# Kernel tuning notes

Measured on AMD Instinct MI355X. Metric: run time of the kernel, lower is better.

Reference implementation:

```python
import jax, jax.numpy as jnp
import numpy as np

BLANK = 512  # blank label index (= vocab_size, last slot of V+1 logits)


def setup_inputs() -> dict:
    key = jax.random.key(0)
    k1, k2, k3, k4 = jax.random.split(key, 4)
    B, T, U, V1 = 16, 256, 64, 513
    logits = jax.random.normal(k1, (B, T, U + 1, V1), dtype=jnp.float32)
    logit_lens = jax.random.randint(k2, (B,), T // 2, T + 1, dtype=jnp.int32)
    y = jax.random.randint(k3, (B, U), 0, BLANK, dtype=jnp.int32)  # labels != blank
    y_lens = jax.random.randint(k4, (B,), U // 2, U + 1, dtype=jnp.int32)
    return {"logits": logits, "logit_lens": logit_lens, "y": y, "y_lens": y_lens}


def _per_seq_loss(logits, y, T_len, U_len):
    # logits: [T, U+1, V+1]; y: [U]
    logp = jax.nn.log_softmax(logits, axis=-1)
    blank_lp = logp[..., BLANK]                                   # [T, U+1]
    # label emission log-prob at (t, u) for emitting y[u]:
    lab_lp = jnp.take_along_axis(logp[:, :-1, :], y[None, :, None], axis=-1)[..., 0]  # [T, U]
    zero = jnp.zeros((1,), logp.dtype)

    def cum(lab_row):
        # c[u] = sum_{j<u} lab_row[j], length U+1
        return jnp.concatenate([zero, jnp.cumsum(lab_row)])

    # alpha recurrence: alpha[t,u] = logaddexp(alpha[t-1,u] + blank_lp[t-1,u],
    #                                          alpha[t,u-1] + lab_lp[t,u-1])
    # Within a row t the u-recursion a[u] = logaddexp(base[u], a[u-1]+lab[u-1])
    # has closed form a[u] = c[u] + logcumsumexp(base - c)[u].
    row0 = cum(lab_lp[0])  # alpha[0, u] = sum of label lps along u axis at t=0

    def step(prev, xs):
        blank_row, lab_row = xs
        base = prev + blank_row          # contribution from alpha[t-1, u]
        c = cum(lab_row)
        a = c + jax.lax.cumlogsumexp(base - c)
        return a, a

    _, rows = jax.lax.scan(step, row0, (blank_lp[:-1], lab_lp[1:]))
    alphas = jnp.concatenate([row0[None], rows], axis=0)  # [T, U+1]
    # final blank transition from (T_len-1, U_len)
    ll = alphas[T_len - 1, U_len] + blank_lp[T_len - 1, U_len]
    return -ll


def reference(logits, logit_lens, y, y_lens):
    per_seq = jax.vmap(_per_seq_loss)(logits, y, logit_lens, y_lens)
    return jnp.mean(per_seq)  # warprnnt 'mean' reduction: average over batch
```

## Files before the change

kernel.cpp:

```cpp
#include <hip/hip_runtime.h>
#include <math.h>

#define BATCH 16
#define TMAX  256
#define UU    64
#define U1    65
#define V1    513
#define BLANKI 512
#define NEG_INF (-INFINITY)

#define BLK_PAD  64
#define LAB_PAD  64
#define BLK_ROWS 384
#define LAB_ROWS 392
#define BLK_SLAB (BLK_ROWS * U1)
#define LAB_SLAB (LAB_ROWS * UU)
#define LOSS_OFF 0
#define BLK_OFF  16
#define LAB_OFF  (BLK_OFF + BATCH * BLK_SLAB)

__device__ __forceinline__ float lae(float x, float y) {
    float m = fmaxf(x, y);
    float z = fminf(x, y);
    return m + __logf(1.0f + __expf(z - m));
}

__global__ __launch_bounds__(1024) void lse_kernel(const float* __restrict__ logits,
                                                   const int* __restrict__ y,
                                                   const int* __restrict__ logit_lens,
                                                   const int* __restrict__ y_lens,
                                                   float* __restrict__ ws) {
    const int wave = (int)((blockIdx.x * 1024u + threadIdx.x) >> 6);
    const int lane = threadIdx.x & 63;
    const int ncells = BATCH * TMAX * U1;
    if (wave >= ncells) return;

    const int u  = wave % U1;
    const int bt = wave / U1;
    const int b  = bt / TMAX;
    const int t  = bt - b * TMAX;
    if (t >= logit_lens[b] || u > y_lens[b]) return;

    const long long base = (long long)wave * V1;

    float v[8];
#pragma unroll
    for (int k = 0; k < 8; ++k) v[k] = logits[base + lane + (k << 6)];
    float vb = (lane == 0) ? logits[base + BLANKI] : NEG_INF;

    float m = vb;
#pragma unroll
    for (int k = 0; k < 8; ++k) m = fmaxf(m, v[k]);
#pragma unroll
    for (int off = 32; off; off >>= 1) m = fmaxf(m, __shfl_xor(m, off));

    float s = (lane == 0) ? __expf(vb - m) : 0.0f;
#pragma unroll
    for (int k = 0; k < 8; ++k) s += __expf(v[k] - m);
#pragma unroll
    for (int off = 32; off; off >>= 1) s += __shfl_xor(s, off);

    const float lse = m + __logf(s);

    if (lane == 0) {
        float* blk = ws + BLK_OFF + b * BLK_SLAB + BLK_PAD * U1;
        blk[t * U1 + u] = vb - lse;
        if (u < UU) {
            float* lab = ws + LAB_OFF + b * LAB_SLAB + LAB_PAD * UU;
            const int label = y[b * UU + u];
            lab[t * UU + u] = logits[base + label] - lse;
        }
    }
}

__global__ __launch_bounds__(64) void alpha_kernel(const float* __restrict__ ws,
                                                   const int* __restrict__ logit_lens,
                                                   const int* __restrict__ y_lens,
                                                   float* __restrict__ losses) {
    const int b    = blockIdx.x;
    const int lane = threadIdx.x;

    const float* __restrict__ blk = ws + BLK_OFF + b * BLK_SLAB + BLK_PAD * U1;
    const float* __restrict__ lab = ws + LAB_OFF + b * LAB_SLAB + LAB_PAD * UU;
    const int Tl = logit_lens[b];
    const int Ul = y_lens[b];
    const int dEnd = Tl - 1 + Ul;

    float a   = (lane == 0) ? 0.0f : NEG_INF;
    float a64 = NEG_INF;
    const int lm1 = (lane == 0) ? 0 : (lane - 1);

    const float* pb   = blk + (0 - lane) * U1 + lane;
    const float* pl   = lab + (1 - lane) * UU + lm1;
    const float* pb64 = blk + (1 - 65) * U1 + 64;
    const float* pl63 = lab + (1 - 64) * UU + 63;

    float bl   = *pb;
    float la   = *pl;
    float bl64 = *pb64;
    float la63 = *pl63;

    int dml = 1 - lane;
    for (int d = 1; d <= dEnd; ++d) {
        pb += U1; pl += UU; pb64 += U1; pl63 += UU;
        const float bl_n   = *pb;
        const float la_n   = *pl;
        const float bl64_n = *pb64;
        const float la63_n = *pl63;

        const float left = __shfl_up(a, 1);
        const float a63b = __shfl(a, 63);

        const float up_in   = a + bl;
        const float left_in = (lane == 0) ? NEG_INF : (left + la);
        const float val     = lae(up_in, left_in);
        a = ((unsigned)dml < (unsigned)Tl) ? val : NEG_INF;

        const float v64 = lae(a64 + bl64, a63b + la63);
        a64 = ((unsigned)(d - 64) < (unsigned)Tl) ? v64 : NEG_INF;

        bl = bl_n; la = la_n; bl64 = bl64_n; la63 = la63_n;
        ++dml;
    }

    const float aU    = (Ul < 64) ? __shfl(a, Ul) : a64;
    const float blast = blk[(Tl - 1) * U1 + Ul];
    if (lane == 0) losses[b] = -(aU + blast);
}

__global__ __launch_bounds__(64) void finalize_kernel(const float* __restrict__ losses,
                                                      float* __restrict__ out) {
    const int lane = threadIdx.x;
    float v = (lane < BATCH) ? losses[lane] : 0.0f;
#pragma unroll
    for (int off = 32; off; off >>= 1) v += __shfl_xor(v, off);
    if (lane == 0) out[0] = v * (1.0f / BATCH);
}

extern "C" void kernel_launch(void* const* d_in, const int* in_sizes, int n_in,
                              void* d_out, int out_size, void* d_ws, size_t ws_size,
                              hipStream_t stream) {
    const float* logits     = (const float*)d_in[0];
    const int*   logit_lens = (const int*)d_in[1];
    const int*   y          = (const int*)d_in[2];
    const int*   y_lens     = (const int*)d_in[3];
    float* out = (float*)d_out;
    float* ws  = (float*)d_ws;

    const int ncells = BATCH * TMAX * U1;
    const int grid = (ncells + 15) / 16;
    lse_kernel<<<grid, 1024, 0, stream>>>(logits, y, logit_lens, y_lens, ws);
    alpha_kernel<<<BATCH, 64, 0, stream>>>(ws, logit_lens, y_lens, ws + LOSS_OFF);
    finalize_kernel<<<1, 64, 0, stream>>>(ws + LOSS_OFF, out);
}
```

Before: 795.1 us.

## Vectorize softmax row loads as float2 and software-pipeline alpha diagonal loads

The LSE kernel now reads each 513-wide row as aligned float2 pairs, with wave parity choosing whether the odd leftover element is the first or the blank one, and it writes the blank and label results from different lanes. The alpha recurrence is unrolled in chunks of 8 diagonals, prefetching the next chunk's blank and label values into registers while the current chunk is computed, and snapshotting the state at the final diagonal. The goal is fewer memory instructions in the bandwidth-bound pass and hidden global-load latency on the serial critical path. The cost is higher register pressure and some extra loads past the end of the sequence, which the workspace padding has to absorb.

```diff
diff --git a/kernel.cpp b/kernel.cpp
--- a/kernel.cpp
+++ b/kernel.cpp
@@ -42,37 +42,43 @@
     if (t >= logit_lens[b] || u > y_lens[b]) return;
 
     const long long base = (long long)wave * V1;
+    const int odd = wave & 1;
+    const long long vbase = base + odd;
 
-    float v[8];
+    float2 v[4];
+    const float2* __restrict__ vp = (const float2*)(logits + vbase);
 #pragma unroll
-    for (int k = 0; k < 8; ++k) v[k] = logits[base + lane + (k << 6)];
-    float vb = (lane == 0) ? logits[base + BLANKI] : NEG_INF;
+    for (int k = 0; k < 4; ++k) v[k] = vp[lane + (k << 6)];
+    const float extra = (lane == 0) ? logits[base + (odd ? 0 : BLANKI)] : NEG_INF;
 
-    float m = vb;
+    float m = extra;
 #pragma unroll
-    for (int k = 0; k < 8; ++k) m = fmaxf(m, v[k]);
+    for (int k = 0; k < 4; ++k) m = fmaxf(m, fmaxf(v[k].x, v[k].y));
 #pragma unroll
     for (int off = 32; off; off >>= 1) m = fmaxf(m, __shfl_xor(m, off));
 
-    float s = (lane == 0) ? __expf(vb - m) : 0.0f;
+    float s = (lane == 0) ? __expf(extra - m) : 0.0f;
 #pragma unroll
-    for (int k = 0; k < 8; ++k) s += __expf(v[k] - m);
+    for (int k = 0; k < 4; ++k) s += __expf(v[k].x - m) + __expf(v[k].y - m);
 #pragma unroll
     for (int off = 32; off; off >>= 1) s += __shfl_xor(s, off);
 
     const float lse = m + __logf(s);
 
-    if (lane == 0) {
+    const float vb_own  = odd ? v[3].y : extra;
+    const int  blk_lane = odd ? 63 : 0;
+    if (lane == blk_lane) {
         float* blk = ws + BLK_OFF + b * BLK_SLAB + BLK_PAD * U1;
-        blk[t * U1 + u] = vb - lse;
-        if (u < UU) {
-            float* lab = ws + LAB_OFF + b * LAB_SLAB + LAB_PAD * UU;
-            const int label = y[b * UU + u];
-            lab[t * UU + u] = logits[base + label] - lse;
-        }
+        blk[t * U1 + u] = vb_own - lse;
+    }
+    if (lane == 1 && u < UU) {
+        float* lab = ws + LAB_OFF + b * LAB_SLAB + LAB_PAD * UU;
+        const int label = y[b * UU + u];
+        lab[t * UU + u] = logits[base + label] - lse;
     }
 }
 
+#define ADEPTH 8
 __global__ __launch_bounds__(64) void alpha_kernel(const float* __restrict__ ws,
                                                    const int* __restrict__ logit_lens,
                                                    const int* __restrict__ y_lens,
@@ -95,35 +101,52 @@
     const float* pb64 = blk + (1 - 65) * U1 + 64;
     const float* pl63 = lab + (1 - 64) * UU + 63;
 
-    float bl   = *pb;
-    float la   = *pl;
-    float bl64 = *pb64;
-    float la63 = *pl63;
-
-    int dml = 1 - lane;
-    for (int d = 1; d <= dEnd; ++d) {
-        pb += U1; pl += UU; pb64 += U1; pl63 += UU;
-        const float bl_n   = *pb;
-        const float la_n   = *pl;
-        const float bl64_n = *pb64;
-        const float la63_n = *pl63;
-
-        const float left = __shfl_up(a, 1);
-        const float a63b = __shfl(a, 63);
-
-        const float up_in   = a + bl;
-        const float left_in = (lane == 0) ? NEG_INF : (left + la);
-        const float val     = lae(up_in, left_in);
-        a = ((unsigned)dml < (unsigned)Tl) ? val : NEG_INF;
-
-        const float v64 = lae(a64 + bl64, a63b + la63);
-        a64 = ((unsigned)(d - 64) < (unsigned)Tl) ? v64 : NEG_INF;
-
-        bl = bl_n; la = la_n; bl64 = bl64_n; la63 = la63_n;
-        ++dml;
+    float qb[ADEPTH], ql[ADEPTH], qb64[ADEPTH], ql63[ADEPTH];
+#pragma unroll
+    for (int k = 0; k < ADEPTH; ++k) {
+        qb[k]   = pb[k * U1];
+        ql[k]   = pl[k * UU];
+        qb64[k] = pb64[k * U1];
+        ql63[k] = pl63[k * UU];
     }
 
-    const float aU    = (Ul < 64) ? __shfl(a, Ul) : a64;
+    float aSnap = NEG_INF, a64Snap = NEG_INF;
+    int dml = 1 - lane;
+    int d   = 1;
+    const int trips = (dEnd + ADEPTH - 1) / ADEPTH;
+    for (int trip = 0; trip < trips; ++trip) {
+        pb += ADEPTH * U1; pl += ADEPTH * UU; pb64 += ADEPTH * U1; pl63 += ADEPTH * UU;
+        float nb[ADEPTH], nl[ADEPTH], nb64[ADEPTH], nl63[ADEPTH];
+#pragma unroll
+        for (int k = 0; k < ADEPTH; ++k) {
+            nb[k]   = pb[k * U1];
+            nl[k]   = pl[k * UU];
+            nb64[k] = pb64[k * U1];
+            nl63[k] = pl63[k * UU];
+        }
+#pragma unroll
+        for (int k = 0; k < ADEPTH; ++k) {
+            const float left = __shfl_up(a, 1);
+            const float a63b = __shfl(a, 63);
+
+            const float up_in   = a + qb[k];
+            const float left_in = (lane == 0) ? NEG_INF : (left + ql[k]);
+            const float val     = lae(up_in, left_in);
+            a = ((unsigned)dml < (unsigned)Tl) ? val : NEG_INF;
+
+            const float v64 = lae(a64 + qb64[k], a63b + ql63[k]);
+            a64 = ((unsigned)(d - 64) < (unsigned)Tl) ? v64 : NEG_INF;
+
+            if (d == dEnd) { aSnap = a; a64Snap = a64; }
+            ++dml; ++d;
+        }
+#pragma unroll
+        for (int k = 0; k < ADEPTH; ++k) {
+            qb[k] = nb[k]; ql[k] = nl[k]; qb64[k] = nb64[k]; ql63[k] = nl63[k];
+        }
+    }
+
+    const float aU    = (Ul < 64) ? __shfl(aSnap, Ul) : a64Snap;
     const float blast = blk[(Tl - 1) * U1 + Ul];
     if (lane == 0) losses[b] = -(aU + blast);
 }
```

Result: faster. 690.1 us (-13.2%).
